# Performance work log

Measured on AMD Instinct MI355X. Metric: run time of the kernel, lower is better.

Reference implementation:

```python
import jax, jax.numpy as jnp
import numpy as np

SPARSITY = 0.01

def quantize(weight, s):
    # ternary quantization: (-s, 0, +s); computed under no_grad in torch
    pos = (weight > s).astype(weight.dtype)
    neg = (weight < -s).astype(weight.dtype)
    return (pos - neg) * s

def setup_inputs() -> dict:
    key = jax.random.key(0)
    k1, k2, k3 = jax.random.split(key, 3)
    B, N, Din, Dout = 8, 2048, 256, 256
    x = jax.random.normal(k1, (B, N, Din), dtype=jnp.float32)
    adj = jax.random.uniform(k2, (B, N, N), dtype=jnp.float32)
    # xavier_uniform_ over (in_dim, out_dim)
    limit = float(np.sqrt(6.0 / (Din + Dout)))
    weight = jax.random.uniform(k3, (Din, Dout), dtype=jnp.float32, minval=-limit, maxval=limit)
    bias = jnp.zeros((Dout,), dtype=jnp.float32)
    return {"x": x, "adj": adj, "weight": weight, "bias": bias}

def reference(x, adj, weight, bias):
    dw = quantize(weight, SPARSITY)          # [Din, Dout] ternary * s
    support = jnp.einsum('bni,io->bno', x, dw)   # [B, N, Dout]
    out = jnp.einsum('bnm,bmo->bno', adj, support) + bias
    return jax.nn.relu(out)
```

## Files before the change

### kernel.cpp

```cpp
#include <hip/hip_runtime.h>
#include <stdint.h>

typedef __attribute__((ext_vector_type(8))) short short8;
typedef __attribute__((ext_vector_type(4))) float f32x4;

static_assert(sizeof(short8) == 16, "frag size");

__device__ __forceinline__ uint16_t f2bf(float f) {
  uint32_t u = __builtin_bit_cast(uint32_t, f);
  u += 0x7fffu + ((u >> 16) & 1u);
  return (uint16_t)(u >> 16);
}

__device__ __forceinline__ short8 pack_bf16x8(f32x4 lo, f32x4 hi) {
  union { uint32_t u[4]; short8 s; } z;
  z.u[0] = (uint32_t)f2bf(lo.x) | ((uint32_t)f2bf(lo.y) << 16);
  z.u[1] = (uint32_t)f2bf(lo.z) | ((uint32_t)f2bf(lo.w) << 16);
  z.u[2] = (uint32_t)f2bf(hi.x) | ((uint32_t)f2bf(hi.y) << 16);
  z.u[3] = (uint32_t)f2bf(hi.z) | ((uint32_t)f2bf(hi.w) << 16);
  return z.s;
}

__device__ __forceinline__ void gload_lds16(const void* g, void* lds_wave_base) {
  __builtin_amdgcn_global_load_lds(
      (__attribute__((address_space(1))) void*)(void*)(g),
      (__attribute__((address_space(3))) void*)(lds_wave_base),
      16, 0, 0);
}


__global__ __launch_bounds__(256) void quant_kernel(const float* __restrict__ w,
                                                    uint16_t* __restrict__ dwT) {
  const int o = blockIdx.x, i = threadIdx.x;
  const float v = w[i * 256 + o];
  const float t = (v > 0.01f) ? 1.0f : ((v < -0.01f) ? -1.0f : 0.0f);
  dwT[o * 256 + (i ^ ((o & 7) << 3))] = f2bf(t);
}

#define SB_A 0
#define SB_B 32768

__global__ __launch_bounds__(256) void support_kernel(const float* __restrict__ x,
                                                      const uint16_t* __restrict__ dwT,
                                                      uint16_t* __restrict__ spt) {
  __shared__ __align__(16) unsigned char smem[65536];
  const int t = threadIdx.x, lane = t & 63, w = t >> 6;
  const int r = lane & 15, q = lane >> 4;
  const int g0 = (blockIdx.x & 255) * 64;
  const int o0 = (blockIdx.x >> 8) * 64;

#pragma unroll
  for (int j = 0; j < 8; ++j) {
    const int id = j * 256 + t;
    const int row = id >> 5, c = id & 31;
    const float* p = x + (size_t)(g0 + row) * 256 + c * 8;
    const f32x4 v0 = *(const f32x4*)p;
    const f32x4 v1 = *(const f32x4*)(p + 4);
    uint4 u;
    u.x = (uint32_t)f2bf(v0.x) | ((uint32_t)f2bf(v0.y) << 16);
    u.y = (uint32_t)f2bf(v0.z) | ((uint32_t)f2bf(v0.w) << 16);
    u.z = (uint32_t)f2bf(v1.x) | ((uint32_t)f2bf(v1.y) << 16);
    u.w = (uint32_t)f2bf(v1.z) | ((uint32_t)f2bf(v1.w) << 16);
    *(uint4*)(smem + SB_A + row * 512 + ((c ^ (row & 7)) << 4)) = u;
  }
#pragma unroll
  for (int j = 0; j < 8; ++j) {
    const int id = j * 256 + t, row = id >> 5, c = id & 31;
    gload_lds16(dwT + (size_t)(o0 + row) * 256 + c * 8,
                smem + SB_B + (size_t)(j * 256 + w * 64) * 16);
  }
  __syncthreads();

  f32x4 acc[4] = {};
#pragma unroll
  for (int h = 0; h < 8; ++h) {
    short8 av, bv[4];
    const int pc = (((h * 4 + q) ^ (r & 7)) << 4);
    av = *(const short8*)(smem + SB_A + (16 * w + r) * 512 + pc);
#pragma unroll
    for (int ni = 0; ni < 4; ++ni)
      bv[ni] = *(const short8*)(smem + SB_B + (16 * ni + r) * 512 + pc);
#pragma unroll
    for (int ni = 0; ni < 4; ++ni)
      acc[ni] = __builtin_amdgcn_mfma_f32_16x16x32_bf16(av, bv[ni], acc[ni], 0, 0, 0);
  }
  __syncthreads();

#pragma unroll
  for (int ni = 0; ni < 4; ++ni) {
    const int ol = 16 * ni + r;
#pragma unroll
    for (int reg = 0; reg < 4; ++reg) {
      const int gl = 16 * w + 4 * q + reg;
      const int gsw = gl ^ ((ol & 7) << 3);
      *(uint16_t*)(smem + (ol * 64 + gsw) * 2) = f2bf(acc[ni][reg] * 0.01f);
    }
  }
  __syncthreads();
#pragma unroll
  for (int it = 0; it < 2; ++it) {
    const int id = it * 256 + t, row = id >> 3, cc = id & 7;
    const uint4 u = *(const uint4*)(smem + (row * 64 + cc * 8) * 2);
    *(uint4*)(spt + (size_t)(o0 + row) * 16384 + g0 + cc * 8) = u;
  }
}

#define MA0 0u
#define MA1 8192u
#define MBB0 16384u
#define MBB1 49152u

__global__ __launch_bounds__(512, 4) void gcn_main_kernel(const float* __restrict__ adj,
                                                          const uint16_t* __restrict__ spt,
                                                          const float* __restrict__ bias,
                                                          float* __restrict__ out) {
  __shared__ __align__(16) unsigned char smem[81920];
  const int t = threadIdx.x, lane = t & 63, wv = t >> 6;
  const int r = lane & 15, q = lane >> 4;
  const int nh = wv >> 2;
  const int oq = wv & 3;
  const int bb = blockIdx.x & 7;
  const int n0 = (blockIdx.x >> 3) * 32;
  const float* adjb = adj + ((size_t)bb * 2048 + n0) * 2048;
  const uint16_t* sptb = spt + (size_t)bb * 2048;

  const int aRowD = 4 * wv + (lane >> 4);
  const int aCl = lane & 15;
  const int aCs = (aCl & 8) | ((aCl & 7) ^ (aRowD & 7));
  const float* aSrc = adjb + (size_t)aRowD * 2048 + aCs * 4;

  const int bRowD = lane >> 3, bCl = lane & 7;

#define STAGE(K0, ABUF, BBUF)                                                  \
  do {                                                                         \
    gload_lds16(aSrc + (K0), smem + (ABUF) + (size_t)wv * 1024);               \
    _Pragma("unroll") for (int j = 0; j < 4; ++j) {                            \
      const int row_ = (4 * wv + j) * 8 + bRowD;                               \
      gload_lds16(sptb + (size_t)row_ * 16384 + (K0) + bCl * 8,                \
                  smem + (BBUF) + (size_t)(4 * wv + j) * 1024);                \
    }                                                                          \
  } while (0)

  f32x4 acc[4] = {};
  const int rr = r & 7;
  const unsigned aRowOff = (nh * 16 + r) * 256;
  const unsigned bRowBase = (oq * 64) * 128;

  STAGE(0, MA0, MBB0);
  __syncthreads();

  for (int kt = 0; kt < 32; ++kt) {
    const unsigned aCur = (kt & 1) ? MA1 : MA0;
    const unsigned bCur = (kt & 1) ? MBB1 : MBB0;
    const unsigned aNxt = (kt & 1) ? MA0 : MA1;
    const unsigned bNxt = (kt & 1) ? MBB0 : MBB1;

    if (kt < 31) STAGE((kt + 1) * 64, aNxt, bNxt);

#pragma unroll
    for (int h = 0; h < 2; ++h) {
      const f32x4 a0 = *(const f32x4*)(smem + aCur + aRowOff +
                                       (h * 8 + ((2 * q) ^ rr)) * 16);
      const f32x4 a1 = *(const f32x4*)(smem + aCur + aRowOff +
                                       (h * 8 + ((2 * q + 1) ^ rr)) * 16);
      const short8 av = pack_bf16x8(a0, a1);
      const int pc = (((h * 4 + q) ^ rr) << 4);
      short8 bv[4];
#pragma unroll
      for (int ni = 0; ni < 4; ++ni)
        bv[ni] = *(const short8*)(smem + bCur + bRowBase + (16 * ni + r) * 128 + pc);
#pragma unroll
      for (int ni = 0; ni < 4; ++ni)
        acc[ni] = __builtin_amdgcn_mfma_f32_16x16x32_bf16(av, bv[ni], acc[ni], 0, 0, 0);
    }
    __syncthreads();
  }

#pragma unroll
  for (int ni = 0; ni < 4; ++ni) {
    const int o = oq * 64 + 16 * ni + r;
    const float bs = bias[o];
#pragma unroll
    for (int reg = 0; reg < 4; ++reg) {
      const int n = n0 + nh * 16 + 4 * q + reg;
      out[((size_t)bb * 2048 + n) * 256 + o] = fmaxf(acc[ni][reg] + bs, 0.0f);
    }
  }
#undef STAGE
}

extern "C" void kernel_launch(void* const* d_in, const int* in_sizes, int n_in,
                              void* d_out, int out_size, void* d_ws, size_t ws_size,
                              hipStream_t stream) {
  const float* x      = (const float*)d_in[0];
  const float* adj    = (const float*)d_in[1];
  const float* weight = (const float*)d_in[2];
  const float* bias   = (const float*)d_in[3];
  float* out = (float*)d_out;

  uint16_t* dwT = (uint16_t*)d_ws;
  uint16_t* spt = (uint16_t*)((char*)d_ws + 131072);

  hipLaunchKernelGGL(quant_kernel,    dim3(256),  dim3(256), 0, stream, weight, dwT);
  hipLaunchKernelGGL(support_kernel,  dim3(1024), dim3(256), 0, stream, x, dwT, spt);
  hipLaunchKernelGGL(gcn_main_kernel, dim3(512),  dim3(512), 0, stream, adj, spt, bias, out);
}
```

Baseline: 244.5 us.

## Triple-buffer main GEMM with 64-row tiles and vmcnt-based waits

Doubles the adj row tile per block from 32 to 64, so each staged spt tile is reused across twice as many output rows and the grid shrinks to 256 blocks. Replaces the double-buffered loop with a three-stage LDS ring that prefetches two k-tiles ahead. The end-of-iteration __syncthreads becomes an explicit s_waitcnt vmcnt plus s_barrier. LDS per block grows to 144KB and launch bounds drop to 2 blocks per CU, so occupancy falls and 256 blocks may not fill all CUs evenly.

```diff
diff --git a/kernel.cpp b/kernel.cpp
--- a/kernel.cpp
+++ b/kernel.cpp
@@ -28,6 +28,7 @@
       16, 0, 0);
 }
 
+#define MEMFENCE() asm volatile("" ::: "memory")
 
 __global__ __launch_bounds__(256) void quant_kernel(const float* __restrict__ w,
                                                     uint16_t* __restrict__ dwT) {
@@ -105,75 +106,96 @@
   }
 }
 
-#define MA0 0u
-#define MA1 8192u
-#define MBB0 16384u
-#define MBB1 49152u
-
-__global__ __launch_bounds__(512, 4) void gcn_main_kernel(const float* __restrict__ adj,
+#define MBUF0 0u
+#define MBUF1 49152u
+#define MBUF2 98304u
+#define MB_BOFF 16384u
+
+__global__ __launch_bounds__(512, 2) void gcn_main_kernel(const float* __restrict__ adj,
                                                           const uint16_t* __restrict__ spt,
                                                           const float* __restrict__ bias,
                                                           float* __restrict__ out) {
-  __shared__ __align__(16) unsigned char smem[81920];
+  __shared__ __align__(16) unsigned char smem[147456];
   const int t = threadIdx.x, lane = t & 63, wv = t >> 6;
   const int r = lane & 15, q = lane >> 4;
-  const int nh = wv >> 2;
+  const int wn = wv >> 2;
   const int oq = wv & 3;
   const int bb = blockIdx.x & 7;
-  const int n0 = (blockIdx.x >> 3) * 32;
+  const int n0 = (blockIdx.x >> 3) * 64;
   const float* adjb = adj + ((size_t)bb * 2048 + n0) * 2048;
   const uint16_t* sptb = spt + (size_t)bb * 2048;
 
-  const int aRowD = 4 * wv + (lane >> 4);
+  const int aRow0 = wv * 8 + (lane >> 4);
   const int aCl = lane & 15;
-  const int aCs = (aCl & 8) | ((aCl & 7) ^ (aRowD & 7));
-  const float* aSrc = adjb + (size_t)aRowD * 2048 + aCs * 4;
-
-  const int bRowD = lane >> 3, bCl = lane & 7;
-
-#define STAGE(K0, ABUF, BBUF)                                                  \
+  const int aCs0 = (aCl & 8) | ((aCl & 7) ^ (aRow0 & 7));
+  const int aCs1 = (aCl & 8) | ((aCl & 7) ^ ((aRow0 + 4) & 7));
+  const float* aSrc0 = adjb + (size_t)aRow0 * 2048 + aCs0 * 4;
+  const float* aSrc1 = adjb + (size_t)(aRow0 + 4) * 2048 + aCs1 * 4;
+  const unsigned aDst0 = (unsigned)(wv * 2) * 1024u;
+  const unsigned aDst1 = aDst0 + 1024u;
+
+  const int bRowIn = lane >> 3, bCl = lane & 7;
+
+#define STAGE(K0, BASE)                                                        \
   do {                                                                         \
-    gload_lds16(aSrc + (K0), smem + (ABUF) + (size_t)wv * 1024);               \
+    gload_lds16(aSrc0 + (K0), smem + (BASE) + aDst0);                          \
+    gload_lds16(aSrc1 + (K0), smem + (BASE) + aDst1);                          \
     _Pragma("unroll") for (int j = 0; j < 4; ++j) {                            \
-      const int row_ = (4 * wv + j) * 8 + bRowD;                               \
+      const int row_ = (4 * wv + j) * 8 + bRowIn;                              \
       gload_lds16(sptb + (size_t)row_ * 16384 + (K0) + bCl * 8,                \
-                  smem + (BBUF) + (size_t)(4 * wv + j) * 1024);                \
+                  smem + (BASE) + MB_BOFF + (size_t)(4 * wv + j) * 1024);      \
     }                                                                          \
+    MEMFENCE();                                                                \
   } while (0)
 
-  f32x4 acc[4] = {};
+  f32x4 acc[2][4] = {};
   const int rr = r & 7;
-  const unsigned aRowOff = (nh * 16 + r) * 256;
-  const unsigned bRowBase = (oq * 64) * 128;
-
-  STAGE(0, MA0, MBB0);
-  __syncthreads();
+
+  STAGE(0, MBUF0);
+  STAGE(64, MBUF1);
+  asm volatile("s_waitcnt vmcnt(6)" ::: "memory");
+  __builtin_amdgcn_s_barrier();
+
+  unsigned bufCur = MBUF0, bufNxt = MBUF1, bufNxt2 = MBUF2;
 
   for (int kt = 0; kt < 32; ++kt) {
-    const unsigned aCur = (kt & 1) ? MA1 : MA0;
-    const unsigned bCur = (kt & 1) ? MBB1 : MBB0;
-    const unsigned aNxt = (kt & 1) ? MA0 : MA1;
-    const unsigned bNxt = (kt & 1) ? MBB0 : MBB1;
-
-    if (kt < 31) STAGE((kt + 1) * 64, aNxt, bNxt);
+    if (kt < 30) STAGE((kt + 2) * 64, bufNxt2);
 
 #pragma unroll
     for (int h = 0; h < 2; ++h) {
-      const f32x4 a0 = *(const f32x4*)(smem + aCur + aRowOff +
-                                       (h * 8 + ((2 * q) ^ rr)) * 16);
-      const f32x4 a1 = *(const f32x4*)(smem + aCur + aRowOff +
-                                       (h * 8 + ((2 * q + 1) ^ rr)) * 16);
-      const short8 av = pack_bf16x8(a0, a1);
+      short8 av[2], bv[4];
+#pragma unroll
+      for (int mi = 0; mi < 2; ++mi) {
+        const int row = wn * 32 + mi * 16 + r;
+        const int g0 = h * 8 + 2 * q;
+        const int c0 = (g0 & 8) | ((g0 & 7) ^ (row & 7));
+        const int c1 = (g0 & 8) | (((g0 + 1) & 7) ^ (row & 7));
+        const f32x4 a0 = *(const f32x4*)(smem + bufCur + row * 256 + c0 * 16);
+        const f32x4 a1 = *(const f32x4*)(smem + bufCur + row * 256 + c1 * 16);
+        av[mi] = pack_bf16x8(a0, a1);
+      }
       const int pc = (((h * 4 + q) ^ rr) << 4);
-      short8 bv[4];
 #pragma unroll
       for (int ni = 0; ni < 4; ++ni)
-        bv[ni] = *(const short8*)(smem + bCur + bRowBase + (16 * ni + r) * 128 + pc);
-#pragma unroll
-      for (int ni = 0; ni < 4; ++ni)
-        acc[ni] = __builtin_amdgcn_mfma_f32_16x16x32_bf16(av, bv[ni], acc[ni], 0, 0, 0);
+        bv[ni] = *(const short8*)(smem + bufCur + MB_BOFF +
+                                  (oq * 64 + 16 * ni + r) * 128 + pc);
+#pragma unroll
+      for (int mi = 0; mi < 2; ++mi)
+#pragma unroll
+        for (int ni = 0; ni < 4; ++ni)
+          acc[mi][ni] = __builtin_amdgcn_mfma_f32_16x16x32_bf16(av[mi], bv[ni],
+                                                                acc[mi][ni], 0, 0, 0);
     }
-    __syncthreads();
+
+    if (kt < 31) {
+      if (kt < 30) {
+        asm volatile("s_waitcnt vmcnt(6)" ::: "memory");
+      } else {
+        asm volatile("s_waitcnt vmcnt(0)" ::: "memory");
+      }
+      __builtin_amdgcn_s_barrier();
+      const unsigned tmp = bufCur; bufCur = bufNxt; bufNxt = bufNxt2; bufNxt2 = tmp;
+    }
   }
 
 #pragma unroll
@@ -181,10 +203,12 @@
     const int o = oq * 64 + 16 * ni + r;
     const float bs = bias[o];
 #pragma unroll
-    for (int reg = 0; reg < 4; ++reg) {
-      const int n = n0 + nh * 16 + 4 * q + reg;
-      out[((size_t)bb * 2048 + n) * 256 + o] = fmaxf(acc[ni][reg] + bs, 0.0f);
-    }
+    for (int mi = 0; mi < 2; ++mi)
+#pragma unroll
+      for (int reg = 0; reg < 4; ++reg) {
+        const int n = n0 + wn * 32 + mi * 16 + 4 * q + reg;
+        out[((size_t)bb * 2048 + n) * 256 + o] = fmaxf(acc[mi][ni][reg] + bs, 0.0f);
+      }
   }
 #undef STAGE
 }
@@ -203,5 +227,5 @@
 
   hipLaunchKernelGGL(quant_kernel,    dim3(256),  dim3(256), 0, stream, weight, dwT);
   hipLaunchKernelGGL(support_kernel,  dim3(1024), dim3(256), 0, stream, x, dwT, spt);
-  hipLaunchKernelGGL(gcn_main_kernel, dim3(512),  dim3(512), 0, stream, adj, spt, bias, out);
-}
+  hipLaunchKernelGGL(gcn_main_kernel, dim3(256),  dim3(512), 0, stream, adj, spt, bias, out);
+}
```

Measured after the change: 228.8 us. 6.4% less time.
